# Performance work log

Measured on AMD Instinct MI355X. Metric: run time of the kernel, lower is better.

The kernel has to match this reference:

```python
import jax, jax.numpy as jnp
import numpy as np
from jax import lax

B, C_IN, T = 64, 16, 8192
HID, OUT = 64, 10
NEW_T = T // 4            # two MaxPool1d(2)
N_NODES = B * NEW_T       # 131072
N_EDGES = 2_097_152       # avg degree 16


def setup_inputs() -> dict:
    key = jax.random.key(0)
    ks = jax.random.split(key, 8)
    x = jax.random.normal(ks[0], (B, C_IN, T), dtype=jnp.float32)
    edge_index = jax.random.randint(ks[1], (2, N_EDGES), 0, N_NODES, dtype=jnp.int32)
    s = 0.05
    return {
        "x": x,
        "edge_index": edge_index,
        "conv1_w": jax.random.normal(ks[2], (16, C_IN, 5), dtype=jnp.float32) * s,
        "conv1_b": jnp.zeros((16,), jnp.float32),
        "conv2_w": jax.random.normal(ks[3], (32, 16, 5), dtype=jnp.float32) * s,
        "conv2_b": jnp.zeros((32,), jnp.float32),
        "gcn1_w": jax.random.normal(ks[4], (32, HID), dtype=jnp.float32) * s,
        "gcn1_b": jnp.zeros((HID,), jnp.float32),
        "gcn2_w": jax.random.normal(ks[5], (HID, HID), dtype=jnp.float32) * s,
        "gcn2_b": jnp.zeros((HID,), jnp.float32),
        "cls_w": jax.random.normal(ks[6], (HID, OUT), dtype=jnp.float32) * s,
        "cls_b": jnp.zeros((OUT,), jnp.float32),
    }


def conv1d(x, w, b):
    # x: [B, Cin, T], w: [Cout, Cin, K], padding=2 -> same length
    y = lax.conv_general_dilated(x, w, window_strides=(1,), padding=[(2, 2)],
                                 dimension_numbers=("NCH", "OIH", "NCH"))
    return y + b[None, :, None]


def maxpool2(x):
    # non-overlapping MaxPool1d(kernel=2) over last dim
    b, c, t = x.shape
    return x.reshape(b, c, t // 2, 2).max(axis=-1)


def gcn_conv(x, edge_index, W, b, n):
    # PyG GCNConv: add self-loops, symmetric normalization, scatter-add aggregate
    row, col = edge_index[0], edge_index[1]   # source j, target i
    loop = jnp.arange(n, dtype=row.dtype)
    row = jnp.concatenate([row, loop])
    col = jnp.concatenate([col, loop])
    deg = jax.ops.segment_sum(jnp.ones(row.shape, x.dtype), col, num_segments=n)
    dis = jnp.where(deg > 0, lax.rsqrt(deg), jnp.zeros_like(deg))
    norm = dis[row] * dis[col]                # [E+N]
    xw = x @ W                                # [N, out]
    msg = xw[row] * norm[:, None]             # gather along edges
    out = jax.ops.segment_sum(msg, col, num_segments=n)
    return out + b


def reference(x, edge_index, conv1_w, conv1_b, conv2_w, conv2_b,
              gcn1_w, gcn1_b, gcn2_w, gcn2_b, cls_w, cls_b):
    h = maxpool2(jax.nn.relu(conv1d(x, conv1_w, conv1_b)))     # [B,16,T/2]
    h = maxpool2(jax.nn.relu(conv1d(h, conv2_w, conv2_b)))     # [B,32,T/4]
    feat = h.transpose(0, 2, 1).reshape(-1, 32)                # [B*new_T, 32]
    n = feat.shape[0]
    g = jax.nn.relu(gcn_conv(feat, edge_index, gcn1_w, gcn1_b, n))
    g = jax.nn.relu(gcn_conv(g, edge_index, gcn2_w, gcn2_b, n))
    pooled = g.reshape(B, -1, HID).mean(axis=1)                # [B, HID]
    return pooled @ cls_w + cls_b                               # [B, OUT]
```

## Files before the change

### kernel.cpp

```cpp
#include <hip/hip_runtime.h>
#include <hip/hip_bf16.h>
#include <hip/hip_fp16.h>

#define BATCH 64
#define C_IN 16
#define T0 8192
#define T1 4096
#define T2 2048
#define N_NODES (BATCH * T2)
#define HID 64
#define NOUT 10

#define NCB 256
#define CB_SHIFT 9
#define CB_TGT 512
#define RCAP 9216
#define PC_EDGES 2048
#define PC_CAP 28

#define PK_RMASK 0x1FFFF

#define EC 1024

#define ZROW N_NODES

#define ROWW 24

#define FP8_SCALE 256.0f
#define FP8_SINV  (1.0f / 256.0f)

typedef __fp16 half8 __attribute__((ext_vector_type(8)));
typedef __fp16 half4v __attribute__((ext_vector_type(4)));
typedef float floatx4 __attribute__((ext_vector_type(4)));
typedef float floatx2 __attribute__((ext_vector_type(2)));

__global__ __launch_bounds__(256) void conv1_kernel(const float* __restrict__ x,
    const float* __restrict__ w, const float* __restrict__ bias,
    __fp16* __restrict__ h1) {
  __shared__ __fp16 xs[528 * ROWW];
  int b = blockIdx.x >> 4;
  int tp0 = (blockIdx.x & 15) * 256;
  int t_base = 2 * tp0 - 8;
  const float* xb = x + (size_t)b * C_IN * T0;
  for (int idx = threadIdx.x; idx < 16 * 132; idx += 256) {
    int ci = idx & 15;
    int c4 = idx >> 4;
    int gt = t_base + c4 * 4;
    float4 v = make_float4(0.f, 0.f, 0.f, 0.f);
    if (gt >= 0 && gt + 4 <= T0) v = *(const float4*)(xb + ci * T0 + gt);
    __fp16* d = xs + (c4 * 4) * ROWW + ci;
    d[0] = (__fp16)v.x;
    d[ROWW] = (__fp16)v.y;
    d[2 * ROWW] = (__fp16)v.z;
    d[3 * ROWW] = (__fp16)v.w;
  }
  int ln = threadIdx.x & 15;
  int q = (threadIdx.x & 63) >> 4;
  int wib = threadIdx.x >> 6;
  half8 wb[3];
#pragma unroll
  for (int ks = 0; ks < 3; ++ks) {
    int kk = ks * 2 + (q >> 1);
#pragma unroll
    for (int j = 0; j < 8; ++j) {
      int ci = (q & 1) * 8 + j;
      float wv = (kk < 5) ? w[(ln * 16 + ci) * 5 + kk] : 0.f;
      wb[ks][j] = (__fp16)wv;
    }
  }
  float bv = bias[ln];
  __syncthreads();
  int qh = q >> 1, qo = (q & 1) * 8;
#pragma unroll 2
  for (int mtl = 0; mtl < 8; ++mtl) {
    int mt = wib * 8 + mtl;
    int posb = mt * 16 + ln + qh + 6;
    half8 a0 = *(const half8*)(xs + posb * ROWW + qo);
    half8 a1 = *(const half8*)(xs + (posb + 2) * ROWW + qo);
    half8 a2 = *(const half8*)(xs + (posb + 4) * ROWW + qo);
    floatx4 c0 = {0.f, 0.f, 0.f, 0.f};
    c0 = __builtin_amdgcn_mfma_f32_16x16x32_f16(a0, wb[0], c0, 0, 0, 0);
    c0 = __builtin_amdgcn_mfma_f32_16x16x32_f16(a1, wb[1], c0, 0, 0, 0);
    c0 = __builtin_amdgcn_mfma_f32_16x16x32_f16(a2, wb[2], c0, 0, 0, 0);
    int tp = tp0 + mt * 8 + q * 2;
    size_t o = ((size_t)b * T1 + tp) * 16 + ln;
    h1[o] = (__fp16)fmaxf(fmaxf(c0[0], c0[1]) + bv, 0.f);
    h1[o + 16] = (__fp16)fmaxf(fmaxf(c0[2], c0[3]) + bv, 0.f);
  }
}

__global__ __launch_bounds__(256) void conv2_gemm1(const __fp16* __restrict__ h1,
    const float* __restrict__ w, const float* __restrict__ bias,
    const float* __restrict__ W1, const float* __restrict__ dis,
    unsigned char* __restrict__ xw) {
  __shared__ __fp16 xs[520 * ROWW];
  __shared__ __fp16 fs[256 * 40];
  int b = blockIdx.x >> 3;
  int tp0 = (blockIdx.x & 7) * 256;
  int t_base = 2 * tp0 - 2;
  for (int idx = threadIdx.x; idx < 520 * 2; idx += 256) {
    int row = idx >> 1;
    int hf = idx & 1;
    int gt = t_base + row;
    half8 v;
#pragma unroll
    for (int j = 0; j < 8; ++j) v[j] = (__fp16)0.f;
    if (gt >= 0 && gt < T1) v = *(const half8*)(h1 + ((size_t)b * T1 + gt) * 16 + hf * 8);
    *(half8*)(xs + row * ROWW + hf * 8) = v;
  }
  int ln = threadIdx.x & 15;
  int q = (threadIdx.x & 63) >> 4;
  int wib = threadIdx.x >> 6;
  half8 wb[2][3];
#pragma unroll
  for (int nt = 0; nt < 2; ++nt)
#pragma unroll
    for (int ks = 0; ks < 3; ++ks) {
      int kk = ks * 2 + (q >> 1);
#pragma unroll
      for (int j = 0; j < 8; ++j) {
        int ci = (q & 1) * 8 + j;
        float wv = (kk < 5) ? w[((nt * 16 + ln) * 16 + ci) * 5 + kk] : 0.f;
        wb[nt][ks][j] = (__fp16)wv;
      }
    }
  float b20 = bias[ln];
  float b21 = bias[16 + ln];
  __syncthreads();
  int qh = q >> 1, qo = (q & 1) * 8;
#pragma unroll 2
  for (int mtl = 0; mtl < 8; ++mtl) {
    int mt = wib * 8 + mtl;
    int posb = mt * 16 + ln + qh;
    half8 a0 = *(const half8*)(xs + posb * ROWW + qo);
    half8 a1 = *(const half8*)(xs + (posb + 2) * ROWW + qo);
    half8 a2 = *(const half8*)(xs + (posb + 4) * ROWW + qo);
    floatx4 c0 = {0.f, 0.f, 0.f, 0.f};
    floatx4 c1 = {0.f, 0.f, 0.f, 0.f};
    c0 = __builtin_amdgcn_mfma_f32_16x16x32_f16(a0, wb[0][0], c0, 0, 0, 0);
    c0 = __builtin_amdgcn_mfma_f32_16x16x32_f16(a1, wb[0][1], c0, 0, 0, 0);
    c0 = __builtin_amdgcn_mfma_f32_16x16x32_f16(a2, wb[0][2], c0, 0, 0, 0);
    c1 = __builtin_amdgcn_mfma_f32_16x16x32_f16(a0, wb[1][0], c1, 0, 0, 0);
    c1 = __builtin_amdgcn_mfma_f32_16x16x32_f16(a1, wb[1][1], c1, 0, 0, 0);
    c1 = __builtin_amdgcn_mfma_f32_16x16x32_f16(a2, wb[1][2], c1, 0, 0, 0);
    int node = wib * 64 + mtl * 8 + q * 2;
    fs[node * 40 + ln] = (__fp16)fmaxf(fmaxf(c0[0], c0[1]) + b20, 0.f);
    fs[(node + 1) * 40 + ln] = (__fp16)fmaxf(fmaxf(c0[2], c0[3]) + b20, 0.f);
    fs[node * 40 + 16 + ln] = (__fp16)fmaxf(fmaxf(c1[0], c1[1]) + b21, 0.f);
    fs[(node + 1) * 40 + 16 + ln] = (__fp16)fmaxf(fmaxf(c1[2], c1[3]) + b21, 0.f);
  }
  half8 bf[4];
#pragma unroll
  for (int t = 0; t < 4; ++t)
#pragma unroll
    for (int j = 0; j < 8; ++j)
      bf[t][j] = (__fp16)W1[(q * 8 + j) * 64 + ln * 4 + t];
  int gnode0 = b * T2 + tp0;
#pragma unroll
  for (int tt = 0; tt < 4; ++tt) {
    int lbase = (wib * 4 + tt) * 16;
    half8 a = *(const half8*)(fs + (lbase + ln) * 40 + q * 8);
    float d[4];
#pragma unroll
    for (int r = 0; r < 4; ++r) d[r] = dis[gnode0 + lbase + q * 4 + r] * FP8_SCALE;
    floatx4 acc[4];
#pragma unroll
    for (int t = 0; t < 4; ++t) {
      floatx4 z = {0.f, 0.f, 0.f, 0.f};
      acc[t] = __builtin_amdgcn_mfma_f32_16x16x32_f16(a, bf[t], z, 0, 0, 0);
    }
#pragma unroll
    for (int r = 0; r < 4; ++r) {
      int u = __builtin_amdgcn_cvt_pk_fp8_f32(acc[0][r] * d[r], acc[1][r] * d[r], 0, 0);
      u = __builtin_amdgcn_cvt_pk_fp8_f32(acc[2][r] * d[r], acc[3][r] * d[r], u, 1);
      *(unsigned*)(xw + (size_t)(gnode0 + lbase + q * 4 + r) * 64 + ln * 4) = (unsigned)u;
    }
  }
}

__global__ __launch_bounds__(256) void partition_pairs(const int* __restrict__ ei, int E,
    int* __restrict__ rcnt, int* __restrict__ gpairs) {
  __shared__ int lcnt[NCB];
  __shared__ int lpk[NCB * PC_CAP];
  if (threadIdx.x < NCB) lcnt[threadIdx.x] = 0;
  __syncthreads();
  int e0 = blockIdx.x * PC_EDGES;
#pragma unroll
  for (int j = 0; j < PC_EDGES / 256; ++j) {
    int e = e0 + j * 256 + threadIdx.x;
    if (e < E) {
      int r = ei[e];
      int c = ei[E + e];
      int cb = c >> CB_SHIFT;
      int pk = r | ((c & (CB_TGT - 1)) << 17);
      int slot = atomicAdd(&lcnt[cb], 1);
      if (slot < PC_CAP) {
        lpk[cb * PC_CAP + slot] = pk;
      } else {
        int pos = atomicAdd(&rcnt[cb], 1);
        if (pos < RCAP) gpairs[(size_t)cb * RCAP + pos] = pk;
      }
    }
  }
  __syncthreads();
  int t = threadIdx.x;
  if (t < NCB) {
    int n = lcnt[t];
    if (n > PC_CAP) n = PC_CAP;
    if (n > 0) {
      int base = atomicAdd(&rcnt[t], n);
      int* dst = gpairs + (size_t)t * RCAP;
      for (int k = 0; k < n; ++k) {
        int p = base + k;
        if (p < RCAP) dst[p] = lpk[t * PC_CAP + k];
      }
    }
  }
}

__global__ __launch_bounds__(512) void build_csr(const int* __restrict__ gpairs,
    const int* __restrict__ rcnt, int* __restrict__ ebuf,
    int* __restrict__ estart, int* __restrict__ ecnt, float* __restrict__ dis) {
  __shared__ int deg[CB_TGT];
  __shared__ int cur[CB_TGT];
  __shared__ int sc[CB_TGT];
  __shared__ int wsum[8];
  int b = blockIdx.x;
  int t = threadIdx.x;
  deg[t] = 0;
  cur[t] = 0;
  __syncthreads();
  int m = rcnt[b];
  if (m > RCAP) m = RCAP;
  const int* reg = gpairs + (size_t)b * RCAP;
  for (int k = t; k < m; k += 512)
    atomicAdd(&deg[(reg[k] >> 17) & (CB_TGT - 1)], 1);
  __syncthreads();
  int d = deg[t];
  int lane = t & 63;
  int wv = t >> 6;
  int sum = d;
#pragma unroll
  for (int off = 1; off < 64; off <<= 1) {
    int v = __shfl_up(sum, off, 64);
    if (lane >= off) sum += v;
  }
  if (lane == 63) wsum[wv] = sum;
  __syncthreads();
  int prefix = 0;
#pragma unroll
  for (int i = 0; i < 8; ++i) prefix += (i < wv) ? wsum[i] : 0;
  int excl = prefix + sum - d;
  int gi = (b << CB_SHIFT) + t;
  int base = b * RCAP;
  estart[gi] = base + excl;
  ecnt[gi] = d;
  dis[gi] = rsqrtf((float)d + 1.0f);
  sc[t] = excl;
  __syncthreads();
  for (int k = t; k < m; k += 512) {
    int p = reg[k];
    int lc = (p >> 17) & (CB_TGT - 1);
    int off = atomicAdd(&cur[lc], 1);
    ebuf[base + sc[lc] + off] = p & PK_RMASK;
  }
}

#define LOADW(dst_, b0_)                                                        \
  _Pragma("unroll")                                                             \
  for (int j = 0; j < 4; ++j) {                                                 \
    unsigned r = (unsigned)sidx[(b0_) + j * 4];                                 \
    dst_[j] = *(const unsigned*)(tab + ((r << 6) + ch4));                       \
  }
#define LOADWT(dst_, stl_, s0_, c_)                                             \
  _Pragma("unroll")                                                             \
  for (int j = 0; j < 4; ++j) {                                                 \
    int k = (s0_) + j * 4 + es;                                                 \
    unsigned r = (unsigned)sidx[(stl_) + k];                                    \
    unsigned off = (k < (c_)) ? ((r << 6) + ch4) : zoff;                        \
    dst_[j] = *(const unsigned*)(tab + off);                                    \
  }
#define CONSW(src_, ALO, AHI)                                                   \
  _Pragma("unroll")                                                             \
  for (int j = 0; j < 4; ++j) {                                                 \
    ALO += __builtin_amdgcn_cvt_pk_f32_fp8(src_[j], 0);                         \
    AHI += __builtin_amdgcn_cvt_pk_f32_fp8(src_[j], 1);                         \
  }
#define GATHER_NODE(c_, stl_, ALO, AHI)                                         \
  {                                                                             \
    int sb_ = (stl_) + es;                                                      \
    int nt_ = ((c_) + 15) >> 4;                                                 \
    int nf_ = (c_) >> 4;                                                        \
    unsigned wa_[4], wb_[4];                                                    \
    if (nt_ > 0) {                                                              \
      if (nf_ > 0) { LOADW(wa_, sb_) } else { LOADWT(wa_, stl_, 0, c_) }        \
    }                                                                           \
    for (int w_ = 0; w_ < nt_; ++w_) {                                          \
      int n_ = w_ + 1;                                                          \
      if (n_ < nt_) {                                                           \
        if (w_ & 1) {                                                           \
          if (n_ < nf_) { LOADW(wa_, sb_ + (n_ << 4)) }                         \
          else { LOADWT(wa_, stl_, n_ << 4, c_) }                               \
        } else {                                                                \
          if (n_ < nf_) { LOADW(wb_, sb_ + (n_ << 4)) }                         \
          else { LOADWT(wb_, stl_, n_ << 4, c_) }                               \
        }                                                                       \
      }                                                                         \
      if (w_ & 1) { CONSW(wb_, ALO, AHI) } else { CONSW(wa_, ALO, AHI) }        \
    }                                                                           \
  }

__global__ __launch_bounds__(256) void agg1_gemm2(const unsigned char* __restrict__ tab,
    const int* __restrict__ ebuf, const int* __restrict__ estart,
    const int* __restrict__ ecnt, const float* __restrict__ dis,
    const float* __restrict__ bias, const float* __restrict__ W2,
    unsigned char* __restrict__ xw2, int N) {
  __shared__ __fp16 g1s[16 * 72];
  __shared__ int sidx[EC + 16];
  __shared__ int sst[16], scn[16];
  int t = threadIdx.x;
  int base16 = blockIdx.x * 16;
  if (t < 16) {
    sst[t] = estart[base16 + t];
    scn[t] = ecnt[base16 + t];
  }
  __syncthreads();
  int span0 = sst[0];
  int total = sst[15] + scn[15] - span0;
  if (total > EC) total = EC;
  for (int k = t; k < total; k += 256) sidx[k] = ebuf[span0 + k];
  __syncthreads();
  int lane = t & 63;
  int es = lane >> 4;
  int ch = lane & 15;
  int wib = t >> 6;
  unsigned ch4 = (unsigned)ch * 4u;
  unsigned zoff = ((unsigned)ZROW << 6) + ch4;
  float4 bv = *(const float4*)(bias + ch * 4);
  half8 b0, b1;
#pragma unroll
  for (int j = 0; j < 8; ++j) {
    b0[j] = (__fp16)W2[((lane >> 4) * 8 + j) * 64 + wib * 16 + (lane & 15)];
    b1[j] = (__fp16)W2[(32 + (lane >> 4) * 8 + j) * 64 + wib * 16 + (lane & 15)];
  }
  unsigned swv[4];
#pragma unroll
  for (int jj = 0; jj < 4; ++jj)
    swv[jj] = *(const unsigned*)(tab + (((unsigned)(base16 + wib * 4 + jj) << 6) + ch4));
#pragma unroll
  for (int jj = 0; jj < 4; ++jj) {
    int il = wib * 4 + jj;
    int i = base16 + il;
    int stl = sst[il] - span0;
    int c = scn[il];
    if (stl + c > EC) c = (EC > stl) ? (EC - stl) : 0;
    float di = dis[i] * FP8_SINV;
    floatx2 aLO = {0.f, 0.f}, aHI = {0.f, 0.f};
    GATHER_NODE(c, stl, aLO, aHI)
    float ax = aLO.x, ay = aLO.y, az = aHI.x, aw = aHI.y;
    ax += __shfl_xor(ax, 16, 64); ax += __shfl_xor(ax, 32, 64);
    ay += __shfl_xor(ay, 16, 64); ay += __shfl_xor(ay, 32, 64);
    az += __shfl_xor(az, 16, 64); az += __shfl_xor(az, 32, 64);
    aw += __shfl_xor(aw, 16, 64); aw += __shfl_xor(aw, 32, 64);
    floatx2 slo = __builtin_amdgcn_cvt_pk_f32_fp8(swv[jj], 0);
    floatx2 shi = __builtin_amdgcn_cvt_pk_f32_fp8(swv[jj], 1);
    if (es == 0) {
      half4v r;
      r[0] = (__fp16)fmaxf((ax + slo.x) * di + bv.x, 0.f);
      r[1] = (__fp16)fmaxf((ay + slo.y) * di + bv.y, 0.f);
      r[2] = (__fp16)fmaxf((az + shi.x) * di + bv.z, 0.f);
      r[3] = (__fp16)fmaxf((aw + shi.y) * di + bv.w, 0.f);
      *(half4v*)(g1s + il * 72 + ch * 4) = r;
    }
  }
  __syncthreads();
  int m = lane & 15;
  int q = lane >> 4;
  half8 a0 = *(const half8*)(g1s + m * 72 + q * 8);
  half8 a1 = *(const half8*)(g1s + m * 72 + 32 + q * 8);
  floatx4 acc = {0.f, 0.f, 0.f, 0.f};
  acc = __builtin_amdgcn_mfma_f32_16x16x32_f16(a0, b0, acc, 0, 0, 0);
  acc = __builtin_amdgcn_mfma_f32_16x16x32_f16(a1, b1, acc, 0, 0, 0);
  float sv[4];
#pragma unroll
  for (int r = 0; r < 4; ++r)
    sv[r] = acc[r] * dis[base16 + q * 4 + r] * FP8_SCALE;
  int u = __builtin_amdgcn_cvt_pk_fp8_f32(sv[0], sv[1], 0, 0);
  u = __builtin_amdgcn_cvt_pk_fp8_f32(sv[2], sv[3], u, 1);
#pragma unroll
  for (int r = 0; r < 4; ++r) {
    int node = base16 + q * 4 + r;
    xw2[(size_t)node * 64 + wib * 16 + m] = (unsigned char)(((unsigned)u) >> (8 * r));
  }
}

__global__ __launch_bounds__(256) void gcn_aggregate_pool(const unsigned char* __restrict__ tab,
    const int* __restrict__ ebuf, const int* __restrict__ estart,
    const int* __restrict__ ecnt, const float* __restrict__ dis,
    const float* __restrict__ bias, float* __restrict__ pool, int N) {
  __shared__ float4 red[4][16];
  __shared__ int sidx[EC + 16];
  __shared__ int sst[16], scn[16];
  int t = threadIdx.x;
  int base16 = blockIdx.x * 16;
  if (t < 16) {
    sst[t] = estart[base16 + t];
    scn[t] = ecnt[base16 + t];
  }
  __syncthreads();
  int span0 = sst[0];
  int total = sst[15] + scn[15] - span0;
  if (total > EC) total = EC;
  for (int k = t; k < total; k += 256) sidx[k] = ebuf[span0 + k];
  __syncthreads();
  int lane = t & 63;
  int es = lane >> 4;
  int ch = lane & 15;
  int wib = t >> 6;
  unsigned ch4 = (unsigned)ch * 4u;
  unsigned zoff = ((unsigned)ZROW << 6) + ch4;
  float4 bv = *(const float4*)(bias + ch * 4);
  unsigned swv[4];
#pragma unroll
  for (int jj = 0; jj < 4; ++jj)
    swv[jj] = *(const unsigned*)(tab + (((unsigned)(base16 + wib * 4 + jj) << 6) + ch4));
  float px = 0.f, py = 0.f, pz = 0.f, pw = 0.f;
#pragma unroll
  for (int jj = 0; jj < 4; ++jj) {
    int il = wib * 4 + jj;
    int i = base16 + il;
    int stl = sst[il] - span0;
    int c = scn[il];
    if (stl + c > EC) c = (EC > stl) ? (EC - stl) : 0;
    float di = dis[i] * FP8_SINV;
    floatx2 aLO = {0.f, 0.f}, aHI = {0.f, 0.f};
    GATHER_NODE(c, stl, aLO, aHI)
    float ax = aLO.x, ay = aLO.y, az = aHI.x, aw = aHI.y;
    ax += __shfl_xor(ax, 16, 64); ax += __shfl_xor(ax, 32, 64);
    ay += __shfl_xor(ay, 16, 64); ay += __shfl_xor(ay, 32, 64);
    az += __shfl_xor(az, 16, 64); az += __shfl_xor(az, 32, 64);
    aw += __shfl_xor(aw, 16, 64); aw += __shfl_xor(aw, 32, 64);
    floatx2 slo = __builtin_amdgcn_cvt_pk_f32_fp8(swv[jj], 0);
    floatx2 shi = __builtin_amdgcn_cvt_pk_f32_fp8(swv[jj], 1);
    px += fmaxf((ax + slo.x) * di + bv.x, 0.f);
    py += fmaxf((ay + slo.y) * di + bv.y, 0.f);
    pz += fmaxf((az + shi.x) * di + bv.z, 0.f);
    pw += fmaxf((aw + shi.y) * di + bv.w, 0.f);
  }
  if (es == 0) red[wib][ch] = make_float4(px, py, pz, pw);
  __syncthreads();
  if (threadIdx.x < 64) {
    int f = threadIdx.x;
    int c4 = f >> 2, j4 = f & 3;
    const float* r0 = (const float*)&red[0][c4];
    const float* r1 = (const float*)&red[1][c4];
    const float* r2 = (const float*)&red[2][c4];
    const float* r3 = (const float*)&red[3][c4];
    float sum = r0[j4] + r1[j4] + r2[j4] + r3[j4];
    int b = (blockIdx.x * 16) >> 11;
    atomicAdd(&pool[b * 64 + f], sum);
  }
}

__global__ __launch_bounds__(64) void classify(const float* __restrict__ pool,
    const float* __restrict__ cw, const float* __restrict__ cb,
    float* __restrict__ out) {
  __shared__ float pl[64];
  int b = blockIdx.x;
  int t = threadIdx.x;
  pl[t] = pool[b * 64 + t] * (1.0f / (float)T2);
  __syncthreads();
  if (t < NOUT) {
    float a = cb[t];
#pragma unroll
    for (int k = 0; k < 64; ++k) a += pl[k] * cw[k * NOUT + t];
    out[b * NOUT + t] = a;
  }
}

extern "C" void kernel_launch(void* const* d_in, const int* in_sizes, int n_in,
                              void* d_out, int out_size, void* d_ws, size_t ws_size,
                              hipStream_t stream) {
  const float* x    = (const float*)d_in[0];
  const int*   ei   = (const int*)d_in[1];
  const float* c1w  = (const float*)d_in[2];
  const float* c1b  = (const float*)d_in[3];
  const float* c2w  = (const float*)d_in[4];
  const float* c2b  = (const float*)d_in[5];
  const float* g1w  = (const float*)d_in[6];
  const float* g1b  = (const float*)d_in[7];
  const float* g2w  = (const float*)d_in[8];
  const float* g2b  = (const float*)d_in[9];
  const float* cw   = (const float*)d_in[10];
  const float* cb   = (const float*)d_in[11];
  float* out = (float*)d_out;
  int E = in_sizes[1] / 2;
  const int N = N_NODES;

  char* ws = (char*)d_ws;
  int*    gpairs = (int*)(ws);
  int*    ebuf   = (int*)(ws + 9437184);
  int*    rcnt   = (int*)(ws + 18874368);
  int*    estart = (int*)(ws + 18878464);
  int*    ecnt   = (int*)(ws + 19402752);
  float*  dis    = (float*)(ws + 19927040);
  float*  pool   = (float*)(ws + 20451328);
  unsigned char* xw  = (unsigned char*)(ws + 20467712);
  unsigned char* xw2 = (unsigned char*)(ws + 37245184);
  __fp16* h1     = (__fp16*)(ws + 54022656);

  hipMemsetAsync(rcnt, 0, NCB * sizeof(int), stream);
  hipMemsetAsync(pool, 0, BATCH * HID * sizeof(float), stream);
  hipMemsetAsync(xw + (size_t)N * 64, 0, 64, stream);
  hipMemsetAsync(xw2 + (size_t)N * 64, 0, 64, stream);

  conv1_kernel<<<dim3(BATCH * 16), dim3(256), 0, stream>>>(x, c1w, c1b, h1);
  partition_pairs<<<dim3((E + PC_EDGES - 1) / PC_EDGES), dim3(256), 0, stream>>>(ei, E, rcnt, gpairs);
  build_csr<<<dim3(NCB), dim3(512), 0, stream>>>(gpairs, rcnt, ebuf, estart, ecnt, dis);

  conv2_gemm1<<<dim3(BATCH * 8), dim3(256), 0, stream>>>(h1, c2w, c2b, g1w, dis, xw);
  agg1_gemm2<<<dim3(N / 16), dim3(256), 0, stream>>>(xw, ebuf, estart, ecnt, dis, g1b, g2w, xw2, N);
  gcn_aggregate_pool<<<dim3(N / 16), dim3(256), 0, stream>>>(xw2, ebuf, estart, ecnt, dis, g2b, pool, N);

  classify<<<dim3(BATCH), dim3(64), 0, stream>>>(pool, cw, cb, out);
}
```

Before: 266.2 us.

## Fuse conv1 and edge partitioning into one launch and fold memsets in

Merges the conv1 kernel and the edge-partition kernel into a single launch. Even blocks run conv1 and odd blocks run partitioning, sharing one overlapping shared-memory buffer. This lets the compute-bound conv work and the atomic-heavy partition work run concurrently. The pool and zero-row memsets move into the first conv1 block, removing three memset calls and one kernel launch. The partition grid size is now tied to the conv1 grid, so it only covers all edges when E is at most 1024*2048.

Measured after the change: 247.6 us. 1.07x faster.

```diff
diff --git a/kernel.cpp b/kernel.cpp
--- a/kernel.cpp
+++ b/kernel.cpp
@@ -34,58 +34,111 @@
 typedef float floatx4 __attribute__((ext_vector_type(4)));
 typedef float floatx2 __attribute__((ext_vector_type(2)));
 
-__global__ __launch_bounds__(256) void conv1_kernel(const float* __restrict__ x,
-    const float* __restrict__ w, const float* __restrict__ bias,
-    __fp16* __restrict__ h1) {
-  __shared__ __fp16 xs[528 * ROWW];
-  int b = blockIdx.x >> 4;
-  int tp0 = (blockIdx.x & 15) * 256;
-  int t_base = 2 * tp0 - 8;
-  const float* xb = x + (size_t)b * C_IN * T0;
-  for (int idx = threadIdx.x; idx < 16 * 132; idx += 256) {
-    int ci = idx & 15;
-    int c4 = idx >> 4;
-    int gt = t_base + c4 * 4;
-    float4 v = make_float4(0.f, 0.f, 0.f, 0.f);
-    if (gt >= 0 && gt + 4 <= T0) v = *(const float4*)(xb + ci * T0 + gt);
-    __fp16* d = xs + (c4 * 4) * ROWW + ci;
-    d[0] = (__fp16)v.x;
-    d[ROWW] = (__fp16)v.y;
-    d[2 * ROWW] = (__fp16)v.z;
-    d[3 * ROWW] = (__fp16)v.w;
-  }
-  int ln = threadIdx.x & 15;
-  int q = (threadIdx.x & 63) >> 4;
-  int wib = threadIdx.x >> 6;
-  half8 wb[3];
-#pragma unroll
-  for (int ks = 0; ks < 3; ++ks) {
-    int kk = ks * 2 + (q >> 1);
-#pragma unroll
-    for (int j = 0; j < 8; ++j) {
-      int ci = (q & 1) * 8 + j;
-      float wv = (kk < 5) ? w[(ln * 16 + ci) * 5 + kk] : 0.f;
-      wb[ks][j] = (__fp16)wv;
-    }
-  }
-  float bv = bias[ln];
-  __syncthreads();
-  int qh = q >> 1, qo = (q & 1) * 8;
+__global__ __launch_bounds__(256) void conv1_partition(
+    const float* __restrict__ x, const float* __restrict__ w,
+    const float* __restrict__ bias, __fp16* __restrict__ h1,
+    const int* __restrict__ ei, int E,
+    int* __restrict__ rcnt, int* __restrict__ gpairs,
+    float* __restrict__ pool, unsigned char* __restrict__ xw,
+    unsigned char* __restrict__ xw2) {
+  __shared__ int smem_i[NCB + NCB * PC_CAP];
+  if ((blockIdx.x & 1) == 0) {
+    __fp16* xs = (__fp16*)smem_i;
+    int bid = blockIdx.x >> 1;
+    int b = bid >> 4;
+    int tp0 = (bid & 15) * 256;
+    if (bid == 0) {
+      for (int k = threadIdx.x; k < BATCH * HID; k += 256) pool[k] = 0.f;
+      if (threadIdx.x < 16) {
+        ((unsigned*)(xw + (size_t)ZROW * 64))[threadIdx.x] = 0u;
+        ((unsigned*)(xw2 + (size_t)ZROW * 64))[threadIdx.x] = 0u;
+      }
+    }
+    int t_base = 2 * tp0 - 8;
+    const float* xb = x + (size_t)b * C_IN * T0;
+    for (int idx = threadIdx.x; idx < 16 * 132; idx += 256) {
+      int ci = idx & 15;
+      int c4 = idx >> 4;
+      int gt = t_base + c4 * 4;
+      float4 v = make_float4(0.f, 0.f, 0.f, 0.f);
+      if (gt >= 0 && gt + 4 <= T0) v = *(const float4*)(xb + ci * T0 + gt);
+      __fp16* d = xs + (c4 * 4) * ROWW + ci;
+      d[0] = (__fp16)v.x;
+      d[ROWW] = (__fp16)v.y;
+      d[2 * ROWW] = (__fp16)v.z;
+      d[3 * ROWW] = (__fp16)v.w;
+    }
+    int ln = threadIdx.x & 15;
+    int q = (threadIdx.x & 63) >> 4;
+    int wib = threadIdx.x >> 6;
+    half8 wb[3];
+#pragma unroll
+    for (int ks = 0; ks < 3; ++ks) {
+      int kk = ks * 2 + (q >> 1);
+#pragma unroll
+      for (int j = 0; j < 8; ++j) {
+        int ci = (q & 1) * 8 + j;
+        float wv = (kk < 5) ? w[(ln * 16 + ci) * 5 + kk] : 0.f;
+        wb[ks][j] = (__fp16)wv;
+      }
+    }
+    float bv = bias[ln];
+    __syncthreads();
+    int qh = q >> 1, qo = (q & 1) * 8;
 #pragma unroll 2
-  for (int mtl = 0; mtl < 8; ++mtl) {
-    int mt = wib * 8 + mtl;
-    int posb = mt * 16 + ln + qh + 6;
-    half8 a0 = *(const half8*)(xs + posb * ROWW + qo);
-    half8 a1 = *(const half8*)(xs + (posb + 2) * ROWW + qo);
-    half8 a2 = *(const half8*)(xs + (posb + 4) * ROWW + qo);
-    floatx4 c0 = {0.f, 0.f, 0.f, 0.f};
-    c0 = __builtin_amdgcn_mfma_f32_16x16x32_f16(a0, wb[0], c0, 0, 0, 0);
-    c0 = __builtin_amdgcn_mfma_f32_16x16x32_f16(a1, wb[1], c0, 0, 0, 0);
-    c0 = __builtin_amdgcn_mfma_f32_16x16x32_f16(a2, wb[2], c0, 0, 0, 0);
-    int tp = tp0 + mt * 8 + q * 2;
-    size_t o = ((size_t)b * T1 + tp) * 16 + ln;
-    h1[o] = (__fp16)fmaxf(fmaxf(c0[0], c0[1]) + bv, 0.f);
-    h1[o + 16] = (__fp16)fmaxf(fmaxf(c0[2], c0[3]) + bv, 0.f);
+    for (int mtl = 0; mtl < 8; ++mtl) {
+      int mt = wib * 8 + mtl;
+      int posb = mt * 16 + ln + qh + 6;
+      half8 a0 = *(const half8*)(xs + posb * ROWW + qo);
+      half8 a1 = *(const half8*)(xs + (posb + 2) * ROWW + qo);
+      half8 a2 = *(const half8*)(xs + (posb + 4) * ROWW + qo);
+      floatx4 c0 = {0.f, 0.f, 0.f, 0.f};
+      c0 = __builtin_amdgcn_mfma_f32_16x16x32_f16(a0, wb[0], c0, 0, 0, 0);
+      c0 = __builtin_amdgcn_mfma_f32_16x16x32_f16(a1, wb[1], c0, 0, 0, 0);
+      c0 = __builtin_amdgcn_mfma_f32_16x16x32_f16(a2, wb[2], c0, 0, 0, 0);
+      int tp = tp0 + mt * 8 + q * 2;
+      size_t o = ((size_t)b * T1 + tp) * 16 + ln;
+      h1[o] = (__fp16)fmaxf(fmaxf(c0[0], c0[1]) + bv, 0.f);
+      h1[o + 16] = (__fp16)fmaxf(fmaxf(c0[2], c0[3]) + bv, 0.f);
+    }
+  } else {
+    int* lcnt = smem_i;
+    int* lpk = smem_i + NCB;
+    int pid = blockIdx.x >> 1;
+    if (threadIdx.x < NCB) lcnt[threadIdx.x] = 0;
+    __syncthreads();
+    int e0 = pid * PC_EDGES;
+#pragma unroll
+    for (int j = 0; j < PC_EDGES / 256; ++j) {
+      int e = e0 + j * 256 + threadIdx.x;
+      if (e < E) {
+        int r = ei[e];
+        int c = ei[E + e];
+        int cb = c >> CB_SHIFT;
+        int pk = r | ((c & (CB_TGT - 1)) << 17);
+        int slot = atomicAdd(&lcnt[cb], 1);
+        if (slot < PC_CAP) {
+          lpk[cb * PC_CAP + slot] = pk;
+        } else {
+          int pos = atomicAdd(&rcnt[cb], 1);
+          if (pos < RCAP) gpairs[(size_t)cb * RCAP + pos] = pk;
+        }
+      }
+    }
+    __syncthreads();
+    int t = threadIdx.x;
+    if (t < NCB) {
+      int n = lcnt[t];
+      if (n > PC_CAP) n = PC_CAP;
+      if (n > 0) {
+        int base = atomicAdd(&rcnt[t], n);
+        int* dst = gpairs + (size_t)t * RCAP;
+        for (int k = 0; k < n; ++k) {
+          int p = base + k;
+          if (p < RCAP) dst[p] = lpk[t * PC_CAP + k];
+        }
+      }
+    }
   }
 }
 
@@ -174,46 +227,6 @@
       int u = __builtin_amdgcn_cvt_pk_fp8_f32(acc[0][r] * d[r], acc[1][r] * d[r], 0, 0);
       u = __builtin_amdgcn_cvt_pk_fp8_f32(acc[2][r] * d[r], acc[3][r] * d[r], u, 1);
       *(unsigned*)(xw + (size_t)(gnode0 + lbase + q * 4 + r) * 64 + ln * 4) = (unsigned)u;
-    }
-  }
-}
-
-__global__ __launch_bounds__(256) void partition_pairs(const int* __restrict__ ei, int E,
-    int* __restrict__ rcnt, int* __restrict__ gpairs) {
-  __shared__ int lcnt[NCB];
-  __shared__ int lpk[NCB * PC_CAP];
-  if (threadIdx.x < NCB) lcnt[threadIdx.x] = 0;
-  __syncthreads();
-  int e0 = blockIdx.x * PC_EDGES;
-#pragma unroll
-  for (int j = 0; j < PC_EDGES / 256; ++j) {
-    int e = e0 + j * 256 + threadIdx.x;
-    if (e < E) {
-      int r = ei[e];
-      int c = ei[E + e];
-      int cb = c >> CB_SHIFT;
-      int pk = r | ((c & (CB_TGT - 1)) << 17);
-      int slot = atomicAdd(&lcnt[cb], 1);
-      if (slot < PC_CAP) {
-        lpk[cb * PC_CAP + slot] = pk;
-      } else {
-        int pos = atomicAdd(&rcnt[cb], 1);
-        if (pos < RCAP) gpairs[(size_t)cb * RCAP + pos] = pk;
-      }
-    }
-  }
-  __syncthreads();
-  int t = threadIdx.x;
-  if (t < NCB) {
-    int n = lcnt[t];
-    if (n > PC_CAP) n = PC_CAP;
-    if (n > 0) {
-      int base = atomicAdd(&rcnt[t], n);
-      int* dst = gpairs + (size_t)t * RCAP;
-      for (int k = 0; k < n; ++k) {
-        int p = base + k;
-        if (p < RCAP) dst[p] = lpk[t * PC_CAP + k];
-      }
     }
   }
 }
@@ -510,12 +523,10 @@
   __fp16* h1     = (__fp16*)(ws + 54022656);
 
   hipMemsetAsync(rcnt, 0, NCB * sizeof(int), stream);
-  hipMemsetAsync(pool, 0, BATCH * HID * sizeof(float), stream);
-  hipMemsetAsync(xw + (size_t)N * 64, 0, 64, stream);
-  hipMemsetAsync(xw2 + (size_t)N * 64, 0, 64, stream);
-
-  conv1_kernel<<<dim3(BATCH * 16), dim3(256), 0, stream>>>(x, c1w, c1b, h1);
-  partition_pairs<<<dim3((E + PC_EDGES - 1) / PC_EDGES), dim3(256), 0, stream>>>(ei, E, rcnt, gpairs);
+
+  conv1_partition<<<dim3(BATCH * 16 * 2), dim3(256), 0, stream>>>(
+      x, c1w, c1b, h1, ei, E, rcnt, gpairs, pool, xw, xw2);
+
   build_csr<<<dim3(NCB), dim3(512), 0, stream>>>(gpairs, rcnt, ebuf, estart, ecnt, dis);
 
   conv2_gemm1<<<dim3(BATCH * 8), dim3(256), 0, stream>>>(h1, c2w, c2b, g1w, dis, xw);
```
